# Performance work log

Hardware: AMD Instinct MI355X
Metric: run time of the kernel (lower is better)

## Reference

```python
import jax, jax.numpy as jnp
import numpy as np

IN_F = 4096
OUT_F = 4096
TOKENS = 8192


def setup_inputs() -> dict:
    key = jax.random.key(0)
    k_x, k_w, k_s, k_b = jax.random.split(key, 4)
    x = jax.random.normal(k_x, (TOKENS, IN_F), dtype=jnp.float32)
    int8_weights = jax.random.randint(k_w, (OUT_F, IN_F), -128, 127, dtype=jnp.int8)
    # per-output-channel scales (symmetric quantization)
    scales = jax.random.uniform(k_s, (OUT_F,), dtype=jnp.float32, minval=0.001, maxval=0.02)
    bias = jax.random.normal(k_b, (1, OUT_F), dtype=jnp.float32)
    return {"input": x, "int8_weights": int8_weights, "scales": scales, "bias": bias}


def reference(input, int8_weights, scales, bias):
    # dequantize: W_fp = int8 * per-row scale, then y = x @ W_fp.T + b
    w = int8_weights.astype(jnp.float32) * scales[:, None]  # [OUT_F, IN_F]
    return jnp.dot(input, w.T) + bias  # [TOKENS, OUT_F]
```

## Files before the change

### kernel.cpp

```cpp
#include <hip/hip_runtime.h>
#include <hip/hip_bf16.h>
#include <stdint.h>

#define TOKENS 8192
#define IN_F   4096
#define OUT_F  4096

typedef __attribute__((ext_vector_type(4))) float f32x4;
typedef __attribute__((ext_vector_type(8))) short bf16x8;
typedef unsigned short u16;

__device__ __forceinline__ u16 f2bf(float f) {
    uint32_t u = __builtin_bit_cast(uint32_t, f);
    u += 0x7fffu + ((u >> 16) & 1u);
    return (u16)(u >> 16);
}

__global__ void __launch_bounds__(256) conv_x_kernel(const float4* __restrict__ in,
                                                     uint4* __restrict__ out, int n8) {
    int i = blockIdx.x * blockDim.x + threadIdx.x;
    const int stride = gridDim.x * blockDim.x;
    for (; i < n8; i += stride) {
        float4 a = in[2 * i], b = in[2 * i + 1];
        union { u16 u[8]; uint4 v; } r;
        r.u[0] = f2bf(a.x); r.u[1] = f2bf(a.y); r.u[2] = f2bf(a.z); r.u[3] = f2bf(a.w);
        r.u[4] = f2bf(b.x); r.u[5] = f2bf(b.y); r.u[6] = f2bf(b.z); r.u[7] = f2bf(b.w);
        out[i] = r.v;
    }
}

__global__ void __launch_bounds__(256) conv_w_kernel(const int4* __restrict__ in,
                                                     uint4* __restrict__ out, int n8) {
    int i = blockIdx.x * blockDim.x + threadIdx.x;
    const int stride = gridDim.x * blockDim.x;
    for (; i < n8; i += stride) {
        int4 a = in[2 * i], b = in[2 * i + 1];
        union { u16 u[8]; uint4 v; } r;
        r.u[0] = f2bf((float)a.x); r.u[1] = f2bf((float)a.y);
        r.u[2] = f2bf((float)a.z); r.u[3] = f2bf((float)a.w);
        r.u[4] = f2bf((float)b.x); r.u[5] = f2bf((float)b.y);
        r.u[6] = f2bf((float)b.z); r.u[7] = f2bf((float)b.w);
        out[i] = r.v;
    }
}

#define BM 128
#define BN 128
#define BK 32

#define GLOAD_LDS16(g, l) __builtin_amdgcn_global_load_lds( \
    (const __attribute__((address_space(1))) void*)(g),     \
    (__attribute__((address_space(3))) void*)(l), 16, 0, 0)

__global__ void __launch_bounds__(256) gemm_kernel(
    const u16* __restrict__ A,
    const u16* __restrict__ B,
    const float* __restrict__ scales,
    const float* __restrict__ bias,
    float* __restrict__ C)
{
    __shared__ u16 sA[BM * BK];
    __shared__ u16 sB[BN * BK];

    const int nbn = OUT_F / BN;
    const int nwg = (TOKENS / BM) * nbn;
    const int bid = blockIdx.x;
    const int wg  = (bid & 7) * (nwg >> 3) + (bid >> 3);
    const int m0  = (wg / nbn) * BM;
    const int n0  = (wg % nbn) * BN;

    const int t    = threadIdx.x;
    const int lane = t & 63;
    const int wid  = t >> 6;
    const int wr   = wid >> 1;
    const int wc   = wid & 1;

    f32x4 acc[4][4] = {};

    const int rowS  = t >> 2;
    const int ksegS = (t & 3) * 8;
    const u16* gA0 = A + (size_t)(m0 + rowS) * IN_F + ksegS;
    const u16* gA1 = A + (size_t)(m0 + 64 + rowS) * IN_F + ksegS;
    const u16* gB0 = B + (size_t)(n0 + rowS) * IN_F + ksegS;
    const u16* gB1 = B + (size_t)(n0 + 64 + rowS) * IN_F + ksegS;
    u16* lA0 = &sA[(wid * 64) * 8];
    u16* lA1 = &sA[(256 + wid * 64) * 8];
    u16* lB0 = &sB[(wid * 64) * 8];
    u16* lB1 = &sB[(256 + wid * 64) * 8];

    const int ra   = wr * 64 + (lane & 15);
    const int rb   = wc * 64 + (lane & 15);
    const int koff = lane >> 4;
    const bf16x8* fA = reinterpret_cast<const bf16x8*>(sA);
    const bf16x8* fB = reinterpret_cast<const bf16x8*>(sB);

    for (int k0 = 0; k0 < IN_F; k0 += BK) {
        __syncthreads();
        GLOAD_LDS16(gA0 + k0, lA0);
        GLOAD_LDS16(gA1 + k0, lA1);
        GLOAD_LDS16(gB0 + k0, lB0);
        GLOAD_LDS16(gB1 + k0, lB1);
        __syncthreads();

        bf16x8 af[4], bfr[4];
#pragma unroll
        for (int mi = 0; mi < 4; ++mi) af[mi]  = fA[(ra + mi * 16) * 4 + koff];
#pragma unroll
        for (int ni = 0; ni < 4; ++ni) bfr[ni] = fB[(rb + ni * 16) * 4 + koff];
#pragma unroll
        for (int mi = 0; mi < 4; ++mi)
#pragma unroll
            for (int ni = 0; ni < 4; ++ni)
                acc[mi][ni] = __builtin_amdgcn_mfma_f32_16x16x32_bf16(
                    af[mi], bfr[ni], acc[mi][ni], 0, 0, 0);
    }

    const int crow0 = (lane >> 4) * 4;
    const int ccol  = lane & 15;
#pragma unroll
    for (int ni = 0; ni < 4; ++ni) {
        const int col = n0 + wc * 64 + ni * 16 + ccol;
        const float s  = scales[col];
        const float bv = bias[col];
#pragma unroll
        for (int mi = 0; mi < 4; ++mi) {
            const int rbase = m0 + wr * 64 + mi * 16 + crow0;
#pragma unroll
            for (int j = 0; j < 4; ++j) {
                C[(size_t)(rbase + j) * OUT_F + col] = acc[mi][ni][j] * s + bv;
            }
        }
    }
}

extern "C" void kernel_launch(void* const* d_in, const int* in_sizes, int n_in,
                              void* d_out, int out_size, void* d_ws, size_t ws_size,
                              hipStream_t stream) {
    const float* x      = (const float*)d_in[0];
    const int*   w8     = (const int*)d_in[1];
    const float* scales = (const float*)d_in[2];
    const float* bias   = (const float*)d_in[3];
    float*       out    = (float*)d_out;

    u16* xbf = (u16*)d_ws;
    u16* wbf = (u16*)((char*)d_ws + (size_t)TOKENS * IN_F * 2);

    conv_x_kernel<<<2048, 256, 0, stream>>>((const float4*)x, (uint4*)xbf,
                                            TOKENS * IN_F / 8);
    conv_w_kernel<<<2048, 256, 0, stream>>>((const int4*)w8, (uint4*)wbf,
                                            OUT_F * IN_F / 8);
    gemm_kernel<<<2048, 256, 0, stream>>>(xbf, wbf, scales, bias, out);
}
```

Baseline: 594.2 us.

## Replace GEMM with 256x256 8-wave ping-pong pipelined kernel with swizzled LDS

Swaps the 128x128 single-buffered BK=32 GEMM for a 256x256-tile, 512-thread kernel with BK=64. It double-buffers A and B in 128KB of dynamic LDS and interleaves global-to-LDS prefetch of later k-tiles with MFMA phases. The kernel also XOR-swizzles LDS offsets to avoid bank conflicts and raises wave priority around MFMA bursts. This aims to hide memory latency and raise MFMA utilisation, at the cost of intricate barrier and waitcnt choreography, which risks subtle race bugs and lower occupancy.

```diff
diff --git a/kernel.cpp b/kernel.cpp
--- a/kernel.cpp
+++ b/kernel.cpp
@@ -5,6 +5,7 @@
 #define TOKENS 8192
 #define IN_F   4096
 #define OUT_F  4096
+#define NT     (IN_F / 64)
 
 typedef __attribute__((ext_vector_type(4))) float f32x4;
 typedef __attribute__((ext_vector_type(8))) short bf16x8;
@@ -44,91 +45,150 @@
     }
 }
 
-#define BM 128
-#define BN 128
-#define BK 32
 
 #define GLOAD_LDS16(g, l) __builtin_amdgcn_global_load_lds( \
     (const __attribute__((address_space(1))) void*)(g),     \
     (__attribute__((address_space(3))) void*)(l), 16, 0, 0)
 
-__global__ void __launch_bounds__(256) gemm_kernel(
+#define SLOT_BYTES 16384
+
+#define PHASE_MMA(QM, QN)                                                      \
+    do {                                                                       \
+        __builtin_amdgcn_s_setprio(1);                                         \
+        _Pragma("unroll")                                                      \
+        for (int i = 0; i < 4; ++i) {                                          \
+            _Pragma("unroll")                                                  \
+            for (int j = 0; j < 2; ++j) {                                      \
+                acc[(QM)*4 + i][(QN)*2 + j] =                                  \
+                    __builtin_amdgcn_mfma_f32_16x16x32_bf16(                   \
+                        a[i][0], b[(QN)*2 + j][0], acc[(QM)*4 + i][(QN)*2 + j], 0, 0, 0); \
+                acc[(QM)*4 + i][(QN)*2 + j] =                                  \
+                    __builtin_amdgcn_mfma_f32_16x16x32_bf16(                   \
+                        a[i][1], b[(QN)*2 + j][1], acc[(QM)*4 + i][(QN)*2 + j], 0, 0, 0); \
+            }                                                                  \
+        }                                                                      \
+        __builtin_amdgcn_s_setprio(0);                                         \
+    } while (0)
+
+__global__ void __launch_bounds__(512, 2) gemm8_kernel(
     const u16* __restrict__ A,
     const u16* __restrict__ B,
     const float* __restrict__ scales,
     const float* __restrict__ bias,
     float* __restrict__ C)
 {
-    __shared__ u16 sA[BM * BK];
-    __shared__ u16 sB[BN * BK];
-
-    const int nbn = OUT_F / BN;
-    const int nwg = (TOKENS / BM) * nbn;
+    extern __shared__ char smem[];
+
+    const int t   = threadIdx.x;
+    const int lane = t & 63;
+    const int w    = t >> 6;
+    const int wm   = w >> 2;
+    const int wn   = w & 3;
+    const int hn   = wn >> 1;
+
+    const int nbn = OUT_F / 256;
+    const int nwg = (TOKENS / 256) * nbn;
     const int bid = blockIdx.x;
     const int wg  = (bid & 7) * (nwg >> 3) + (bid >> 3);
-    const int m0  = (wg / nbn) * BM;
-    const int n0  = (wg % nbn) * BN;
-
-    const int t    = threadIdx.x;
-    const int lane = t & 63;
-    const int wid  = t >> 6;
-    const int wr   = wid >> 1;
-    const int wc   = wid & 1;
-
-    f32x4 acc[4][4] = {};
-
-    const int rowS  = t >> 2;
-    const int ksegS = (t & 3) * 8;
-    const u16* gA0 = A + (size_t)(m0 + rowS) * IN_F + ksegS;
-    const u16* gA1 = A + (size_t)(m0 + 64 + rowS) * IN_F + ksegS;
-    const u16* gB0 = B + (size_t)(n0 + rowS) * IN_F + ksegS;
-    const u16* gB1 = B + (size_t)(n0 + 64 + rowS) * IN_F + ksegS;
-    u16* lA0 = &sA[(wid * 64) * 8];
-    u16* lA1 = &sA[(256 + wid * 64) * 8];
-    u16* lB0 = &sB[(wid * 64) * 8];
-    u16* lB1 = &sB[(256 + wid * 64) * 8];
-
-    const int ra   = wr * 64 + (lane & 15);
-    const int rb   = wc * 64 + (lane & 15);
-    const int koff = lane >> 4;
-    const bf16x8* fA = reinterpret_cast<const bf16x8*>(sA);
-    const bf16x8* fB = reinterpret_cast<const bf16x8*>(sB);
-
-    for (int k0 = 0; k0 < IN_F; k0 += BK) {
-        __syncthreads();
-        GLOAD_LDS16(gA0 + k0, lA0);
-        GLOAD_LDS16(gA1 + k0, lA1);
-        GLOAD_LDS16(gB0 + k0, lB0);
-        GLOAD_LDS16(gB1 + k0, lB1);
-        __syncthreads();
-
-        bf16x8 af[4], bfr[4];
-#pragma unroll
-        for (int mi = 0; mi < 4; ++mi) af[mi]  = fA[(ra + mi * 16) * 4 + koff];
-#pragma unroll
-        for (int ni = 0; ni < 4; ++ni) bfr[ni] = fB[(rb + ni * 16) * 4 + koff];
-#pragma unroll
-        for (int mi = 0; mi < 4; ++mi)
-#pragma unroll
-            for (int ni = 0; ni < 4; ++ni)
-                acc[mi][ni] = __builtin_amdgcn_mfma_f32_16x16x32_bf16(
-                    af[mi], bfr[ni], acc[mi][ni], 0, 0, 0);
-    }
-
-    const int crow0 = (lane >> 4) * 4;
-    const int ccol  = lane & 15;
+    const int m0  = (wg / nbn) * 256;
+    const int n0  = (wg % nbn) * 256;
+
+    const int rowLane = w * 8 + (lane >> 3);
+    const int ksegOff = ((lane & 7) ^ (((lane >> 5) & 1) << 1)) * 8;
+    char* const ldsW  = smem + w * 1024;
+
+    const int laneRow = lane & 15;
+    const int kb0 = ((lane >> 4) * 16) ^ ((lane & 4) << 3);
+    const int kb1 = kb0 + 64;
+
+    f32x4 acc[8][4] = {};
+    bf16x8 a[4][2], b[4][2];
+
+    auto STAGE = [&](const u16* mat, int rowBase, int half, int tt, int slotIdx) {
+        const u16* s0 = mat + (size_t)(rowBase + half * 128 + rowLane) * IN_F
+                            + tt * 64 + ksegOff;
+        char* dst = ldsW + slotIdx * SLOT_BYTES;
+        GLOAD_LDS16(s0, dst);
+        GLOAD_LDS16(s0 + (size_t)64 * IN_F, dst + 8192);
+    };
+    auto RDA = [&](const char* aS, int qm) {
+#pragma unroll
+        for (int mi = 0; mi < 4; ++mi) {
+            const int rb = (qm * 64 + mi * 16 + laneRow) * 128;
+            a[mi][0] = *(const bf16x8*)(aS + rb + kb0);
+            a[mi][1] = *(const bf16x8*)(aS + rb + kb1);
+        }
+    };
+    auto RDB = [&](const char* bS) {
+#pragma unroll
+        for (int ni = 0; ni < 4; ++ni) {
+            const int rb = ((wn & 1) * 64 + ni * 16 + laneRow) * 128;
+            b[ni][0] = *(const bf16x8*)(bS + rb + kb0);
+            b[ni][1] = *(const bf16x8*)(bS + rb + kb1);
+        }
+    };
+
+    STAGE(B, n0, 0, 0, 1*4 + 0*2 + 0);
+    STAGE(B, n0, 1, 0, 1*4 + 1*2 + 0);
+    STAGE(A, m0, 0, 0, 0*4 + 0*2 + 0);
+    STAGE(A, m0, 1, 0, 0*4 + 1*2 + 0);
+    STAGE(B, n0, 0, 1, 1*4 + 0*2 + 1);
+    STAGE(B, n0, 1, 1, 1*4 + 1*2 + 1);
+    STAGE(A, m0, 0, 1, 0*4 + 0*2 + 1);
+    asm volatile("s_waitcnt vmcnt(6)" ::: "memory");
+    __builtin_amdgcn_sched_barrier(0);
+    __builtin_amdgcn_s_barrier();
+
+    for (int kt = 0; kt < NT; ++kt) {
+        const int p  = kt & 1, np = p ^ 1;
+        const char* aS = smem + (0*4 + wm * 2 + p) * SLOT_BYTES;
+        const char* bS = smem + (1*4 + hn * 2 + p) * SLOT_BYTES;
+        const int t1 = (kt + 1 < NT) ? kt + 1 : NT - 1;
+        const int t2 = (kt + 2 < NT) ? kt + 2 : NT - 1;
+
+        RDA(aS, 0);
+        RDB(bS);
+        STAGE(A, m0, 1, t1, 0*4 + 1*2 + np);
+        __builtin_amdgcn_s_barrier();
+        PHASE_MMA(0, 0);
+        asm volatile("s_waitcnt lgkmcnt(0)" ::: "memory");
+        __builtin_amdgcn_sched_barrier(0);
+        __builtin_amdgcn_s_barrier();
+
+        STAGE(B, n0, 0, t2, 1*4 + 0*2 + p);
+        __builtin_amdgcn_s_barrier();
+        PHASE_MMA(0, 1);
+        __builtin_amdgcn_s_barrier();
+
+        RDA(aS, 1);
+        STAGE(B, n0, 1, t2, 1*4 + 1*2 + p);
+        __builtin_amdgcn_s_barrier();
+        PHASE_MMA(1, 0);
+        asm volatile("s_waitcnt lgkmcnt(0)" ::: "memory");
+        __builtin_amdgcn_sched_barrier(0);
+        __builtin_amdgcn_s_barrier();
+
+        STAGE(A, m0, 0, t2, 0*4 + 0*2 + p);
+        __builtin_amdgcn_s_barrier();
+        PHASE_MMA(1, 1);
+        asm volatile("s_waitcnt vmcnt(6)" ::: "memory");
+        __builtin_amdgcn_sched_barrier(0);
+        __builtin_amdgcn_s_barrier();
+    }
+
+    const int crow = (lane >> 4) * 4;
+    const int ccol = lane & 15;
 #pragma unroll
     for (int ni = 0; ni < 4; ++ni) {
-        const int col = n0 + wc * 64 + ni * 16 + ccol;
+        const int col = n0 + wn * 64 + ni * 16 + ccol;
         const float s  = scales[col];
         const float bv = bias[col];
 #pragma unroll
-        for (int mi = 0; mi < 4; ++mi) {
-            const int rbase = m0 + wr * 64 + mi * 16 + crow0;
-#pragma unroll
-            for (int j = 0; j < 4; ++j) {
+        for (int mi = 0; mi < 8; ++mi) {
+            const int rbase = m0 + wm * 128 + mi * 16 + crow;
+#pragma unroll
+            for (int j = 0; j < 4; ++j)
                 C[(size_t)(rbase + j) * OUT_F + col] = acc[mi][ni][j] * s + bv;
-            }
         }
     }
 }
@@ -149,5 +209,13 @@
                                             TOKENS * IN_F / 8);
     conv_w_kernel<<<2048, 256, 0, stream>>>((const int4*)w8, (uint4*)wbf,
                                             OUT_F * IN_F / 8);
-    gemm_kernel<<<2048, 256, 0, stream>>>(xbf, wbf, scales, bias, out);
-}
+
+    static bool attr_set = []() {
+        hipFuncSetAttribute(reinterpret_cast<const void*>(gemm8_kernel),
+                            hipFuncAttributeMaxDynamicSharedMemorySize, 131072);
+        return true;
+    }();
+    (void)attr_set;
+
+    gemm8_kernel<<<512, 512, 131072, stream>>>(xbf, wbf, scales, bias, out);
+}
```

Result: faster. 516.8 us (-13.0%).
